# Optimization experiments

Hardware: AMD Instinct MI355X
Metric: run time of the kernel (lower is better)

The kernel has to match this reference:

```python
import jax, jax.numpy as jnp
import numpy as np

# Config constants (from DeepSeekConfig / init_kwargs)
NUM_EXPERTS = 6
VAR_EXPERTS = 4
FIXED_EXPERTS = NUM_EXPERTS - VAR_EXPERTS  # 2
TOP_K = 2
D_MODEL = 1024
D_FF = 4 * D_MODEL
LN_EPS = 1e-5


def setup_inputs() -> dict:
    key = jax.random.key(0)
    ks = jax.random.split(key, 6)
    B, S = 2, 2048
    x = jax.random.normal(ks[0], (B, S, D_MODEL), dtype=jnp.float32)
    router_W = jax.random.normal(ks[1], (D_MODEL, VAR_EXPERTS), dtype=jnp.float32) * 0.02
    # stacked expert FFN params: (E, D, 4D) and (E, 4D, D)
    W1 = jax.random.normal(ks[2], (NUM_EXPERTS, D_MODEL, D_FF), dtype=jnp.float32) * 0.02
    b1 = jnp.zeros((NUM_EXPERTS, D_FF), dtype=jnp.float32)
    W2 = jax.random.normal(ks[3], (NUM_EXPERTS, D_FF, D_MODEL), dtype=jnp.float32) * 0.02
    b2 = jnp.zeros((NUM_EXPERTS, D_MODEL), dtype=jnp.float32)
    ln_gamma = jnp.ones((D_MODEL,), dtype=jnp.float32)
    ln_beta = jnp.zeros((D_MODEL,), dtype=jnp.float32)
    return {"x": x, "router_W": router_W, "W1": W1, "b1": b1, "W2": W2,
            "b2": b2, "ln_gamma": ln_gamma, "ln_beta": ln_beta}


def reference(x, router_W, W1, b1, W2, b2, ln_gamma, ln_beta):
    B, S, D = x.shape
    # router over the VARIABLE experts only
    router_logits = jnp.einsum('bsd,de->bse', x, router_W)          # (B,S,VAR)
    router_probs = jax.nn.softmax(router_logits, axis=-1)
    _, topk_idx = jax.lax.top_k(router_probs, TOP_K)                 # (B,S,K)
    adj_idx = topk_idx + FIXED_EXPERTS                               # global expert ids in [FIXED, NUM)

    # dense per-expert FFN on all tokens: experts[e](x) = gelu(x@W1[e]+b1[e]) @ W2[e] + b2[e]
    h = jnp.einsum('bsd,edf->ebsf', x, W1) + b1[:, None, None, :]    # (E,B,S,4D)
    h = jax.nn.gelu(h, approximate=False)                            # torch F.gelu default = exact
    all_out = jnp.einsum('ebsf,efd->ebsd', h, W2) + b2[:, None, None, :]  # (E,B,S,D)

    # fixed experts: all of experts[0:FIXED] applied to every token
    fixed_sum = all_out[:FIXED_EXPERTS].sum(axis=0)                  # (B,S,D)

    # variable experts: per-token gather of the top-k selected experts
    b_ix = jnp.arange(B)[:, None, None]
    s_ix = jnp.arange(S)[None, :, None]
    var = all_out[adj_idx, b_ix, s_ix, :]                            # (B,S,K,D)

    # cat along expert slot dim then mean == sum / (FIXED + K); topk probs unused (plain mean)
    combined = (fixed_sum + var.sum(axis=2)) / (FIXED_EXPERTS + TOP_K)

    # LayerNorm (biased variance, eps=1e-5)
    mu = combined.mean(axis=-1, keepdims=True)
    v = combined.var(axis=-1, keepdims=True)
    out = (combined - mu) / jnp.sqrt(v + LN_EPS) * ln_gamma + ln_beta
    return out, router_logits
```

## Files before the change

### kernel.cpp

```cpp
#include <hip/hip_runtime.h>
#include <cstdint>
#include <cstddef>

#define D_MODEL 1024
#define D_FF 4096
#define NTOK 4096
#define LN_EPS 1e-5f

typedef __bf16 bf16x8 __attribute__((ext_vector_type(8)));
typedef float f32x4 __attribute__((ext_vector_type(4)));
typedef unsigned short u16x4 __attribute__((ext_vector_type(4)));
typedef unsigned short u16x8 __attribute__((ext_vector_type(8)));

static __device__ __forceinline__ unsigned short f2bf(float f) {
    union { float f; unsigned u; } v; v.f = f;
    unsigned r = v.u + 0x7fffu + ((v.u >> 16) & 1u);
    return (unsigned short)(r >> 16);
}

static __device__ __forceinline__ float b2f(unsigned short u) {
    union { unsigned u; float f; } v; v.u = (unsigned)u << 16;
    return v.f;
}

static __device__ __forceinline__ float gelu_fast(float x) {
    float x2 = x * x;
    float a2 = x * __builtin_fmaf(-0.1029432f, x2, -2.3022084f);
    float e = __builtin_amdgcn_exp2f(a2);
    return x * __builtin_amdgcn_rcpf(1.0f + e);
}

static __device__ __forceinline__ void gload16(const void* g, void* l) {
    __builtin_amdgcn_global_load_lds(
        (const __attribute__((address_space(1))) void*)g,
        (__attribute__((address_space(3))) void*)l, 16, 0, 0);
}

static __device__ __forceinline__ void seg_of(const int* cnt, int seg[4], int pc[4]) {
    int o = 2 * NTOK;
    #pragma unroll
    for (int e = 0; e < 4; ++e) {
        int c = cnt[e * 32];
        pc[e] = (c + 255) & ~255;
        seg[e] = o;
        o += pc[e];
    }
}

__global__ __launch_bounds__(256) void convx_kernel(const float* __restrict__ x,
                                                    unsigned short* __restrict__ xb) {
    int idx = blockIdx.x * 256 + threadIdx.x;
    f32x4 v = *(const f32x4*)&x[(size_t)idx * 4];
    u16x4 b;
    b[0] = f2bf(v[0]); b[1] = f2bf(v[1]); b[2] = f2bf(v[2]); b[3] = f2bf(v[3]);
    *(u16x4*)&xb[(size_t)idx * 4] = b;
}

__global__ __launch_bounds__(256) void transpose_kernel(const float* __restrict__ W,
                                                        unsigned short* __restrict__ Wt,
                                                        int K, int N) {
    __shared__ unsigned short t[64][65];
    int k0 = blockIdx.y * 64, n0 = blockIdx.x * 64;
    const float* We = W + (size_t)blockIdx.z * K * N;
    unsigned short* Wte = Wt + (size_t)blockIdx.z * K * N;
    #pragma unroll
    for (int i = 0; i < 4; ++i) {
        int idx = threadIdx.x + i * 256;
        int kr = idx >> 4, c4 = idx & 15;
        f32x4 v = *(const f32x4*)&We[(size_t)(k0 + kr) * N + n0 + c4 * 4];
        #pragma unroll
        for (int j = 0; j < 4; ++j) t[c4 * 4 + j][kr] = f2bf(v[j]);
    }
    __syncthreads();
    #pragma unroll
    for (int i = 0; i < 2; ++i) {
        int idx = threadIdx.x + i * 256;
        int nr = idx >> 3, ck = idx & 7;
        u16x8 w;
        #pragma unroll
        for (int j = 0; j < 8; ++j) w[j] = t[nr][ck * 8 + j];
        *(u16x8*)&Wte[(size_t)(n0 + nr) * K + k0 + ck * 8] = w;
    }
}

__global__ __launch_bounds__(256) void router_kernel(
        const float* __restrict__ x, const float* __restrict__ rW,
        float* __restrict__ logits, int* __restrict__ selpk,
        int* __restrict__ slotpk, int* __restrict__ cnt, int* __restrict__ list) {
    __shared__ int se[8];
    __shared__ int sslot[8];
    int wid = threadIdx.x >> 6, lane = threadIdx.x & 63;
    int t = blockIdx.x * 4 + wid;
    const float* xr = x + (size_t)t * D_MODEL;
    float a0 = 0.f, a1 = 0.f, a2 = 0.f, a3 = 0.f;
    for (int d = lane; d < D_MODEL; d += 64) {
        float xv = xr[d];
        const float* w = rW + d * 4;
        a0 += xv * w[0]; a1 += xv * w[1]; a2 += xv * w[2]; a3 += xv * w[3];
    }
    #pragma unroll
    for (int off = 32; off; off >>= 1) {
        a0 += __shfl_xor(a0, off); a1 += __shfl_xor(a1, off);
        a2 += __shfl_xor(a2, off); a3 += __shfl_xor(a3, off);
    }
    if (lane == 0) {
        float l[4] = {a0, a1, a2, a3};
        logits[t * 4 + 0] = a0; logits[t * 4 + 1] = a1;
        logits[t * 4 + 2] = a2; logits[t * 4 + 3] = a3;
        int e0 = 0; float b = l[0];
        #pragma unroll
        for (int e = 1; e < 4; ++e) if (l[e] > b) { b = l[e]; e0 = e; }
        int e1 = -1; float b2 = -1e30f;
        #pragma unroll
        for (int e = 0; e < 4; ++e) {
            if (e == e0) continue;
            if (l[e] > b2) { b2 = l[e]; e1 = e; }
        }
        se[wid * 2] = e0; se[wid * 2 + 1] = e1;
    }
    __syncthreads();
    if (threadIdx.x == 0) {
        int cnts[4] = {0, 0, 0, 0}, base[4];
        #pragma unroll
        for (int k = 0; k < 8; ++k) cnts[se[k]]++;
        #pragma unroll
        for (int e = 0; e < 4; ++e)
            if (cnts[e]) base[e] = atomicAdd(&cnt[e * 32], cnts[e]);
        int run[4] = {0, 0, 0, 0};
        #pragma unroll
        for (int k = 0; k < 8; ++k) {
            int e = se[k];
            int s = base[e] + run[e]++;
            sslot[k] = s;
            list[e * NTOK + s] = blockIdx.x * 4 + (k >> 1);
        }
    }
    __syncthreads();
    if (lane == 0) {
        selpk[t] = se[wid * 2] | (se[wid * 2 + 1] << 8);
        slotpk[t] = sslot[wid * 2] | (sslot[wid * 2 + 1] << 16);
    }
}

template<int GELU>
__global__ __launch_bounds__(256) void gemm_kernel(
        const unsigned short* __restrict__ A, const unsigned short* __restrict__ B,
        const float* __restrict__ bias, int bias_stride, int ldo,
        unsigned short* __restrict__ out,
        const int* __restrict__ cnt, const int* __restrict__ list, int K) {
    __shared__ unsigned short As[128 * 64];
    __shared__ unsigned short Bs[128 * 64];
    const int e = blockIdx.z;
    const int tid = threadIdx.x, lane = tid & 63, wid = tid >> 6;
    int ecnt = NTOK, rowbase;
    if (e < 2) {
        rowbase = e * NTOK + blockIdx.y * 128;
    } else {
        int seg[4], pc[4];
        seg_of(cnt, seg, pc);
        int ev = e - 2;
        ecnt = cnt[ev * 32];
        if ((int)blockIdx.y * 128 >= pc[ev]) return;
        rowbase = seg[ev] + blockIdx.y * 128;
    }
    const int n0 = blockIdx.x * 128;
    const unsigned short* Be = B + (size_t)e * (D_FF * D_MODEL);

    const unsigned short* asrc[4];
    const unsigned short* bsrc[4];
    #pragma unroll
    for (int j = 0; j < 4; ++j) {
        int row = (wid * 4 + j) * 8 + (lane >> 3);
        int kc = lane & 7;
        size_t arow;
        if (GELU) {
            int s = blockIdx.y * 128 + row;
            if (e < 2) arow = (size_t)s;
            else       arow = (size_t)((s < ecnt) ? list[(e - 2) * NTOK + s] : 0);
        } else {
            arow = (size_t)(rowbase + row);
        }
        asrc[j] = A + arow * K + ((kc ^ (row & 7)) << 3);
        bsrc[j] = Be + (size_t)(n0 + row) * K + ((kc ^ (row & 7)) << 3);
    }
    const int wm = (wid >> 1) * 64, wn = (wid & 1) * 64;
    const int rl = lane & 15, kq = lane >> 4;

    float bv[4];
    #pragma unroll
    for (int ni = 0; ni < 4; ++ni)
        bv[ni] = bias[(size_t)e * bias_stride + n0 + wn + ni * 16 + rl];

    f32x4 acc[4][4];
    #pragma unroll
    for (int mi = 0; mi < 4; ++mi)
        #pragma unroll
        for (int ni = 0; ni < 4; ++ni) acc[mi][ni] = (f32x4)(bv[ni]);

    for (int kb = 0; kb < K; kb += 64) {
        #pragma unroll
        for (int j = 0; j < 4; ++j) gload16(asrc[j] + kb, &As[(wid * 4 + j) * 512]);
        #pragma unroll
        for (int j = 0; j < 4; ++j) gload16(bsrc[j] + kb, &Bs[(wid * 4 + j) * 512]);
        asm volatile("s_waitcnt vmcnt(0)" ::: "memory");
        __syncthreads();
        #pragma unroll
        for (int kk = 0; kk < 2; ++kk) {
            int kof = kk * 32 + kq * 8;
            bf16x8 a[4], b[4];
            #pragma unroll
            for (int mi = 0; mi < 4; ++mi) {
                int r = wm + mi * 16 + rl;
                a[mi] = *(const bf16x8*)&As[r * 64 + (kof ^ ((r & 7) << 3))];
            }
            #pragma unroll
            for (int ni = 0; ni < 4; ++ni) {
                int r = wn + ni * 16 + rl;
                b[ni] = *(const bf16x8*)&Bs[r * 64 + (kof ^ ((r & 7) << 3))];
            }
            #pragma unroll
            for (int mi = 0; mi < 4; ++mi)
                #pragma unroll
                for (int ni = 0; ni < 4; ++ni)
                    acc[mi][ni] = __builtin_amdgcn_mfma_f32_16x16x32_bf16(
                        a[mi], b[ni], acc[mi][ni], 0, 0, 0);
        }
        __syncthreads();
    }

    #pragma unroll
    for (int ni = 0; ni < 4; ++ni) {
        int c = n0 + wn + ni * 16 + rl;
        #pragma unroll
        for (int mi = 0; mi < 4; ++mi) {
            #pragma unroll
            for (int jp = 0; jp < 2; ++jp) {
                float g0 = acc[mi][ni][jp * 2 + 0];
                float g1 = acc[mi][ni][jp * 2 + 1];
                if (GELU) { g0 = gelu_fast(g0); g1 = gelu_fast(g1); }
                unsigned pk;
                asm("v_cvt_pk_bf16_f32 %0, %1, %2" : "=v"(pk) : "v"(g0), "v"(g1));
                int r = wm + mi * 16 + kq * 4 + jp * 2;
                unsigned short* p = out + (size_t)(rowbase + r) * ldo + c;
                p[0]   = (unsigned short)pk;
                p[ldo] = (unsigned short)(pk >> 16);
            }
        }
    }
}

__global__ __launch_bounds__(256) void pass3_kernel(
        const unsigned short* __restrict__ oslab, const int* __restrict__ selpk,
        const int* __restrict__ slotpk, const int* __restrict__ cnt,
        const float* __restrict__ gamma, const float* __restrict__ beta,
        float* __restrict__ out) {
    int t = blockIdx.x;
    int seg[4], pc[4];
    seg_of(cnt, seg, pc);
    int sp = selpk[t], sl = slotpk[t];
    int e0 = sp & 0xff, e1 = (sp >> 8) & 0xff;
    int s0 = sl & 0xffff, s1 = (sl >> 16) & 0xffff;
    const unsigned short* p0 = oslab + (size_t)t * D_MODEL;
    const unsigned short* p1 = oslab + (size_t)(NTOK + t) * D_MODEL;
    const unsigned short* p2 = oslab + (size_t)(seg[e0] + s0) * D_MODEL;
    const unsigned short* p3 = oslab + (size_t)(seg[e1] + s1) * D_MODEL;
    float c[4];
    float sum = 0.f, sq = 0.f;
    #pragma unroll
    for (int i = 0; i < 4; ++i) {
        int d = threadIdx.x + i * 256;
        float v = (b2f(p0[d]) + b2f(p1[d]) + b2f(p2[d]) + b2f(p3[d])) * 0.25f;
        c[i] = v; sum += v; sq += v * v;
    }
    #pragma unroll
    for (int off = 32; off; off >>= 1) {
        sum += __shfl_xor(sum, off);
        sq  += __shfl_xor(sq, off);
    }
    __shared__ float red[8];
    int lane = threadIdx.x & 63, wid = threadIdx.x >> 6;
    if (lane == 0) { red[wid] = sum; red[4 + wid] = sq; }
    __syncthreads();
    sum = red[0] + red[1] + red[2] + red[3];
    sq  = red[4] + red[5] + red[6] + red[7];
    float mean = sum * (1.0f / 1024.0f);
    float var = sq * (1.0f / 1024.0f) - mean * mean;
    float inv = rsqrtf(var + LN_EPS);
    #pragma unroll
    for (int i = 0; i < 4; ++i) {
        int d = threadIdx.x + i * 256;
        out[(size_t)t * D_MODEL + d] = (c[i] - mean) * inv * gamma[d] + beta[d];
    }
}

extern "C" void kernel_launch(void* const* d_in, const int* in_sizes, int n_in,
                              void* d_out, int out_size, void* d_ws, size_t ws_size,
                              hipStream_t stream) {
    const float* x   = (const float*)d_in[0];
    const float* rW  = (const float*)d_in[1];
    const float* W1  = (const float*)d_in[2];
    const float* b1  = (const float*)d_in[3];
    const float* W2  = (const float*)d_in[4];
    const float* b2  = (const float*)d_in[5];
    const float* gam = (const float*)d_in[6];
    const float* bet = (const float*)d_in[7];
    float* out = (float*)d_out;
    float* logits = out + (size_t)NTOK * D_MODEL;

    char* ws = (char*)d_ws;
    int* cnt    = (int*)ws;
    int* selpk  = (int*)(ws + 0x1000);
    int* slotpk = (int*)(ws + 0x6000);
    int* list   = (int*)(ws + 0xB000);
    unsigned short* xb    = (unsigned short*)(ws + 0x20000);
    unsigned short* W1t   = (unsigned short*)(ws + 0x820000);
    unsigned short* W2t   = (unsigned short*)(ws + 0x3820000);
    unsigned short* oslab = (unsigned short*)(ws + 0x6820000);
    unsigned short* h     = (unsigned short*)(ws + 0x8A20000);

    convx_kernel<<<NTOK * D_MODEL / 4 / 256, 256, 0, stream>>>(x, xb);
    transpose_kernel<<<dim3(D_FF / 64, D_MODEL / 64, 6), 256, 0, stream>>>(W1, W1t, D_MODEL, D_FF);
    transpose_kernel<<<dim3(D_MODEL / 64, D_FF / 64, 6), 256, 0, stream>>>(W2, W2t, D_FF, D_MODEL);
    hipMemsetAsync(cnt, 0, 512, stream);
    router_kernel<<<NTOK / 4, 256, 0, stream>>>(x, rW, logits, selpk, slotpk, cnt, list);

    gemm_kernel<1><<<dim3(D_FF / 128, 32, 6), 256, 0, stream>>>(
        xb, W1t, b1, D_FF, D_FF, h, cnt, list, D_MODEL);
    gemm_kernel<0><<<dim3(D_MODEL / 128, 32, 6), 256, 0, stream>>>(
        h, W2t, b2, D_MODEL, D_MODEL, oslab, cnt, list, D_FF);

    pass3_kernel<<<NTOK, 256, 0, stream>>>(oslab, selpk, slotpk, cnt, gam, bet, out);
}
```

Baseline: 489.1 us.

## Double-buffer GEMM LDS tiles and fuse x bf16 conversion into router

After: 549.3 us. 1.12x slower.

```diff
diff --git a/kernel.cpp b/kernel.cpp
--- a/kernel.cpp
+++ b/kernel.cpp
@@ -45,15 +45,6 @@
         seg[e] = o;
         o += pc[e];
     }
-}
-
-__global__ __launch_bounds__(256) void convx_kernel(const float* __restrict__ x,
-                                                    unsigned short* __restrict__ xb) {
-    int idx = blockIdx.x * 256 + threadIdx.x;
-    f32x4 v = *(const f32x4*)&x[(size_t)idx * 4];
-    u16x4 b;
-    b[0] = f2bf(v[0]); b[1] = f2bf(v[1]); b[2] = f2bf(v[2]); b[3] = f2bf(v[3]);
-    *(u16x4*)&xb[(size_t)idx * 4] = b;
 }
 
 __global__ __launch_bounds__(256) void transpose_kernel(const float* __restrict__ W,
@@ -86,17 +77,31 @@
 __global__ __launch_bounds__(256) void router_kernel(
         const float* __restrict__ x, const float* __restrict__ rW,
         float* __restrict__ logits, int* __restrict__ selpk,
-        int* __restrict__ slotpk, int* __restrict__ cnt, int* __restrict__ list) {
+        int* __restrict__ slotpk, int* __restrict__ cnt, int* __restrict__ list,
+        unsigned short* __restrict__ xb) {
     __shared__ int se[8];
     __shared__ int sslot[8];
     int wid = threadIdx.x >> 6, lane = threadIdx.x & 63;
     int t = blockIdx.x * 4 + wid;
     const float* xr = x + (size_t)t * D_MODEL;
+    unsigned short* xbr = xb + (size_t)t * D_MODEL;
     float a0 = 0.f, a1 = 0.f, a2 = 0.f, a3 = 0.f;
-    for (int d = lane; d < D_MODEL; d += 64) {
-        float xv = xr[d];
-        const float* w = rW + d * 4;
-        a0 += xv * w[0]; a1 += xv * w[1]; a2 += xv * w[2]; a3 += xv * w[3];
+    #pragma unroll
+    for (int i = 0; i < 4; ++i) {
+        int d4 = lane + i * 64;
+        f32x4 xv = *(const f32x4*)&xr[d4 * 4];
+        u16x4 bo;
+        #pragma unroll
+        for (int j = 0; j < 4; ++j) {
+            float xj = xv[j];
+            f32x4 wv = *(const f32x4*)&rW[(d4 * 4 + j) * 4];
+            a0 = __builtin_fmaf(xj, wv[0], a0);
+            a1 = __builtin_fmaf(xj, wv[1], a1);
+            a2 = __builtin_fmaf(xj, wv[2], a2);
+            a3 = __builtin_fmaf(xj, wv[3], a3);
+            bo[j] = f2bf(xj);
+        }
+        *(u16x4*)&xbr[d4 * 4] = bo;
     }
     #pragma unroll
     for (int off = 32; off; off >>= 1) {
@@ -148,8 +153,8 @@
         const float* __restrict__ bias, int bias_stride, int ldo,
         unsigned short* __restrict__ out,
         const int* __restrict__ cnt, const int* __restrict__ list, int K) {
-    __shared__ unsigned short As[128 * 64];
-    __shared__ unsigned short Bs[128 * 64];
+    __shared__ unsigned short As[2][128 * 64];
+    __shared__ unsigned short Bs[2][128 * 64];
     const int e = blockIdx.z;
     const int tid = threadIdx.x, lane = tid & 63, wid = tid >> 6;
     int ecnt = NTOK, rowbase;
@@ -197,13 +202,24 @@
         #pragma unroll
         for (int ni = 0; ni < 4; ++ni) acc[mi][ni] = (f32x4)(bv[ni]);
 
-    for (int kb = 0; kb < K; kb += 64) {
-        #pragma unroll
-        for (int j = 0; j < 4; ++j) gload16(asrc[j] + kb, &As[(wid * 4 + j) * 512]);
-        #pragma unroll
-        for (int j = 0; j < 4; ++j) gload16(bsrc[j] + kb, &Bs[(wid * 4 + j) * 512]);
-        asm volatile("s_waitcnt vmcnt(0)" ::: "memory");
-        __syncthreads();
+    const int nt = K / 64;
+
+    #define STAGE(bf, t)                                                        \
+        {                                                                       \
+            _Pragma("unroll")                                                   \
+            for (int j_ = 0; j_ < 4; ++j_) {                                    \
+                gload16(asrc[j_] + (t) * 64, &As[bf][(wid * 4 + j_) * 512]);    \
+                gload16(bsrc[j_] + (t) * 64, &Bs[bf][(wid * 4 + j_) * 512]);    \
+            }                                                                   \
+        }
+
+    STAGE(0, 0);
+    asm volatile("s_waitcnt vmcnt(0)" ::: "memory");
+    __syncthreads();
+
+    for (int t = 0; t < nt; ++t) {
+        const int cur = t & 1;
+        if (t + 1 < nt) STAGE(cur ^ 1, t + 1);
         #pragma unroll
         for (int kk = 0; kk < 2; ++kk) {
             int kof = kk * 32 + kq * 8;
@@ -211,12 +227,12 @@
             #pragma unroll
             for (int mi = 0; mi < 4; ++mi) {
                 int r = wm + mi * 16 + rl;
-                a[mi] = *(const bf16x8*)&As[r * 64 + (kof ^ ((r & 7) << 3))];
+                a[mi] = *(const bf16x8*)&As[cur][r * 64 + (kof ^ ((r & 7) << 3))];
             }
             #pragma unroll
             for (int ni = 0; ni < 4; ++ni) {
                 int r = wn + ni * 16 + rl;
-                b[ni] = *(const bf16x8*)&Bs[r * 64 + (kof ^ ((r & 7) << 3))];
+                b[ni] = *(const bf16x8*)&Bs[cur][r * 64 + (kof ^ ((r & 7) << 3))];
             }
             #pragma unroll
             for (int mi = 0; mi < 4; ++mi)
@@ -225,8 +241,12 @@
                     acc[mi][ni] = __builtin_amdgcn_mfma_f32_16x16x32_bf16(
                         a[mi], b[ni], acc[mi][ni], 0, 0, 0);
         }
-        __syncthreads();
-    }
+        if (t + 1 < nt) {
+            asm volatile("s_waitcnt vmcnt(0)" ::: "memory");
+            __syncthreads();
+        }
+    }
+    #undef STAGE
 
     #pragma unroll
     for (int ni = 0; ni < 4; ++ni) {
@@ -318,11 +338,10 @@
     unsigned short* oslab = (unsigned short*)(ws + 0x6820000);
     unsigned short* h     = (unsigned short*)(ws + 0x8A20000);
 
-    convx_kernel<<<NTOK * D_MODEL / 4 / 256, 256, 0, stream>>>(x, xb);
+    hipMemsetAsync(cnt, 0, 512, stream);
+    router_kernel<<<NTOK / 4, 256, 0, stream>>>(x, rW, logits, selpk, slotpk, cnt, list, xb);
     transpose_kernel<<<dim3(D_FF / 64, D_MODEL / 64, 6), 256, 0, stream>>>(W1, W1t, D_MODEL, D_FF);
     transpose_kernel<<<dim3(D_MODEL / 64, D_FF / 64, 6), 256, 0, stream>>>(W2, W2t, D_FF, D_MODEL);
-    hipMemsetAsync(cnt, 0, 512, stream);
-    router_kernel<<<NTOK / 4, 256, 0, stream>>>(x, rW, logits, selpk, slotpk, cnt, list);
 
     gemm_kernel<1><<<dim3(D_FF / 128, 32, 6), 256, 0, stream>>>(
         xb, W1t, b1, D_FF, D_FF, h, cnt, list, D_MODEL);
```
